# Kernel tuning notes

Hardware: AMD Instinct MI355X
Metric: run time of the kernel (lower is better)

The kernel has to match this reference:

```python
import jax, jax.numpy as jnp
import numpy as np

B, HH, WW, C, HEADS = 8, 56, 56, 384, 6
DIM_OUT = 384


def _upsample2x_bilinear(x):
    # x: [..., m, n] -> [..., 2m, 2n]; matches torch F.interpolate bilinear align_corners=False
    m, n = x.shape[-2], x.shape[-1]
    def coords(inn):
        c = (jnp.arange(2 * inn) + 0.5) / 2.0 - 0.5
        c = jnp.clip(c, 0.0, inn - 1)
        i0 = jnp.floor(c).astype(jnp.int32)
        i1 = jnp.minimum(i0 + 1, inn - 1)
        return i0, i1, (c - i0).astype(x.dtype)
    i0, i1, wy = coords(m)
    j0, j1, wx = coords(n)
    rows = x[..., i0, :] * (1 - wy)[:, None] + x[..., i1, :] * wy[:, None]
    return rows[..., :, j0] * (1 - wx) + rows[..., :, j1] * wx


def setup_inputs() -> dict:
    key = jax.random.key(0)
    ks = jax.random.split(key, 12)
    inp = {
        'x': jax.random.normal(ks[0], (B, HH * WW, C), jnp.float32),
        'res_attn': jax.random.normal(ks[1], (B, HEADS, (HH // 4) * (WW // 4), (HH // 2) * (WW // 2)), jnp.float32),
        'conv_q_w': jax.random.normal(ks[2], (C, 1, 3, 3), jnp.float32) * 0.05,
        'ln_g': jnp.ones((C,), jnp.float32),
        'ln_b': jnp.zeros((C,), jnp.float32),
        'wq': jax.random.normal(ks[3], (DIM_OUT, C), jnp.float32) * 0.02,
        'wk': jax.random.normal(ks[4], (DIM_OUT, C), jnp.float32) * 0.02,
        'wv': jax.random.normal(ks[5], (DIM_OUT, C), jnp.float32) * 0.02,
        'w_proj': jax.random.normal(ks[6], (DIM_OUT, DIM_OUT), jnp.float32) * 0.02,
        'b_proj': jnp.zeros((DIM_OUT,), jnp.float32),
        'w_fuse': jax.random.normal(ks[7], (HEADS, 2 * HEADS, 1, 1), jnp.float32) * 0.1,
        'b_fuse': jnp.zeros((HEADS,), jnp.float32),
        'h': HH,
        'w': WW,
    }
    return inp


def reference(x, res_attn, conv_q_w, ln_g, ln_b, wq, wk, wv, w_proj, b_proj, w_fuse, b_fuse, h, w):
    Bz, _, Cc = x.shape
    heads = w_fuse.shape[0]
    xi = x.transpose(0, 2, 1).reshape(Bz, Cc, h, w)  # b c h w
    # conv_proj_q: depthwise conv k3 s2 p1 (no bias), then LayerNorm
    q = jax.lax.conv_general_dilated(
        xi, conv_q_w, (2, 2), ((1, 1), (1, 1)),
        dimension_numbers=('NCHW', 'OIHW', 'NCHW'), feature_group_count=Cc)
    hq, wq2 = q.shape[2], q.shape[3]
    q = q.reshape(Bz, Cc, hq * wq2).transpose(0, 2, 1)  # b t c
    mu = q.mean(-1, keepdims=True)
    var = ((q - mu) ** 2).mean(-1, keepdims=True)
    q = (q - mu) / jnp.sqrt(var + 1e-5) * ln_g + ln_b
    # conv_proj_k/v: avg pool k2 s2 p0
    kv = xi.reshape(Bz, Cc, h // 2, 2, w // 2, 2).mean(axis=(3, 5))
    kv = kv.reshape(Bz, Cc, (h // 2) * (w // 2)).transpose(0, 2, 1)  # b t c
    dim_out = wq.shape[0]
    dh = dim_out // heads
    def split(t):
        return t.reshape(Bz, t.shape[1], heads, dh).transpose(0, 2, 1, 3)
    qh = split(q @ wq.T)
    kh = split(kv @ wk.T)
    vh = split(kv @ wv.T)
    scale = dim_out ** -0.5
    attn_score = jnp.einsum('bhlk,bhtk->bhlt', qh, kh) * scale  # [B,H,L,T]
    sh, sw = h // 4, w // 4
    a = res_attn.shape[-1]
    rx = res_attn[:, :, :sh * sw, :]
    rx = rx.reshape(Bz * heads, sh * sw, a).transpose(0, 2, 1).reshape(Bz * heads, a, sh, sw)
    rx = _upsample2x_bilinear(rx)  # (b h) a 2sh 2sw
    rx = rx.reshape(Bz, heads, a, 4 * sh * sw).transpose(0, 1, 3, 2)  # b h L a
    cat = jnp.concatenate([attn_score, rx], axis=1)  # [B, 2H, L, T]
    attn_score = jnp.einsum('bclt,oc->bolt', cat, w_fuse[:, :, 0, 0]) + b_fuse[None, :, None, None]
    attn = jax.nn.softmax(attn_score, axis=-1)
    out = jnp.einsum('bhlt,bhtv->bhlv', attn, vh)
    out = out.transpose(0, 2, 1, 3).reshape(Bz, -1, dim_out)
    return out @ w_proj.T + b_proj
```

## Files before the change

kernel.cpp:

```cpp
#include <hip/hip_runtime.h>

typedef unsigned int uint;
typedef unsigned short ushort_t;
typedef short bf16x8 __attribute__((ext_vector_type(8)));
typedef float f32x4 __attribute__((ext_vector_type(4)));

__device__ __forceinline__ ushort_t f2bf(float f) {
  uint u = __builtin_bit_cast(uint, f);
  u += 0x7fffu + ((u >> 16) & 1u);
  return (ushort_t)(u >> 16);
}
__device__ __forceinline__ float bf2f(ushort_t s) {
  return __builtin_bit_cast(float, (uint)s << 16);
}
__device__ __forceinline__ bf16x8 ld_frag(const ushort_t* p) {
  return __builtin_bit_cast(bf16x8, *(const uint4*)p);
}

__global__ __launch_bounds__(384) void k_convln(
    const float* __restrict__ x, const float* __restrict__ wc,
    const float* __restrict__ g, const float* __restrict__ bb,
    ushort_t* __restrict__ qout, ushort_t* __restrict__ kvout)
{
  const int b  = blockIdx.x / 784;
  const int t  = blockIdx.x % 784;
  const int oy = t / 28, ox = t % 28;
  const int c  = threadIdx.x;
  const float* xb = x + (size_t)b * 3136 * 384 + c;
  float acc = 0.f, pv = 0.f;
  #pragma unroll
  for (int ky = 0; ky < 3; ky++) {
    const int iy = 2 * oy - 1 + ky;
    const bool yok = (iy >= 0) & (iy < 56);
    #pragma unroll
    for (int kx = 0; kx < 3; kx++) {
      const int ix = 2 * ox - 1 + kx;
      if (yok & (ix >= 0) & (ix < 56)) {
        const float xv = xb[(size_t)(iy * 56 + ix) * 384];
        acc += wc[c * 9 + ky * 3 + kx] * xv;
        if ((ky >= 1) & (kx >= 1)) pv += xv;
      }
    }
  }
  kvout[((size_t)b * 784 + t) * 384 + c] = f2bf(pv * 0.25f);
  float s = acc, s2 = acc * acc;
  #pragma unroll
  for (int off = 32; off >= 1; off >>= 1) {
    s  += __shfl_xor(s,  off);
    s2 += __shfl_xor(s2, off);
  }
  __shared__ float ps[6], ps2[6];
  if ((c & 63) == 0) { ps[c >> 6] = s; ps2[c >> 6] = s2; }
  __syncthreads();
  float S = 0.f, S2 = 0.f;
  #pragma unroll
  for (int i = 0; i < 6; i++) { S += ps[i]; S2 += ps2[i]; }
  const float mu  = S * (1.f / 384.f);
  const float var = S2 * (1.f / 384.f) - mu * mu;
  const float inv = rsqrtf(var + 1e-5f);
  qout[((size_t)b * 784 + t) * 384 + c] = f2bf((acc - mu) * inv * g[c] + bb[c]);
}

__global__ __launch_bounds__(256) void k_wcvt(
    const float* __restrict__ a, const float* __restrict__ b,
    const float* __restrict__ c, const float* __restrict__ d,
    ushort_t* __restrict__ oa, ushort_t* __restrict__ ob,
    ushort_t* __restrict__ oc, ushort_t* __restrict__ od)
{
  const int i = blockIdx.x * 256 + threadIdx.x;
  if (i < 147456) {
    oa[i] = f2bf(a[i]); ob[i] = f2bf(b[i]);
    oc[i] = f2bf(c[i]); od[i] = f2bf(d[i]);
  }
}

template<int MODE>
__global__ __launch_bounds__(256) void k_gemm(
    const ushort_t* __restrict__ X, const ushort_t* __restrict__ W,
    const float* __restrict__ bias, void* __restrict__ Y)
{
  __shared__ ushort_t As[128][40];
  __shared__ ushort_t Bs[128][40];
  const int tid = threadIdx.x, w = tid >> 6, lane = tid & 63;
  const int quad = lane >> 4, r = lane & 15;
  const int m0 = blockIdx.y * 128, n0 = blockIdx.x * 128;
  const int wm = w >> 1, wn = w & 1;
  const int lr = tid >> 2, lc = (tid & 3) << 3;
  const ushort_t* xp = X + (size_t)(m0 + lr) * 384 + lc;
  const ushort_t* wp = W + (size_t)(n0 + lr) * 384 + lc;
  f32x4 acc[4][4] = {};
  for (int k0 = 0; k0 < 384; k0 += 32) {
    __syncthreads();
    *(uint4*)&As[lr][lc]      = *(const uint4*)(xp + k0);
    *(uint4*)&As[lr + 64][lc] = *(const uint4*)(xp + (size_t)64 * 384 + k0);
    *(uint4*)&Bs[lr][lc]      = *(const uint4*)(wp + k0);
    *(uint4*)&Bs[lr + 64][lc] = *(const uint4*)(wp + (size_t)64 * 384 + k0);
    __syncthreads();
    bf16x8 af[4], bf_[4];
    #pragma unroll
    for (int mt = 0; mt < 4; mt++) af[mt]  = *(const bf16x8*)&As[wm * 64 + mt * 16 + r][quad * 8];
    #pragma unroll
    for (int nt = 0; nt < 4; nt++) bf_[nt] = *(const bf16x8*)&Bs[wn * 64 + nt * 16 + r][quad * 8];
    #pragma unroll
    for (int mt = 0; mt < 4; mt++)
      #pragma unroll
      for (int nt = 0; nt < 4; nt++)
        acc[mt][nt] = __builtin_amdgcn_mfma_f32_16x16x32_bf16(af[mt], bf_[nt], acc[mt][nt], 0, 0, 0);
  }
  #pragma unroll
  for (int mt = 0; mt < 4; mt++) {
    #pragma unroll
    for (int nt = 0; nt < 4; nt++) {
      #pragma unroll
      for (int i = 0; i < 4; i++) {
        const int row = m0 + wm * 64 + mt * 16 + quad * 4 + i;
        const int col = n0 + wn * 64 + nt * 16 + r;
        const float v = acc[mt][nt][i];
        if constexpr (MODE == 2) {
          ((float*)Y)[(size_t)row * 384 + col] = v + bias[col];
        } else if constexpr (MODE == 0) {
          ((ushort_t*)Y)[(size_t)row * 384 + col] = f2bf(v);
        } else {
          const int bb = row / 784, tt = row % 784;
          ((ushort_t*)Y)[((size_t)bb * 384 + col) * 784 + tt] = f2bf(v);
        }
      }
    }
  }
}

__global__ __launch_bounds__(256) void k_qk(
    const ushort_t* __restrict__ Qb, const ushort_t* __restrict__ Kb,
    ushort_t* __restrict__ S)
{
  const int tid = threadIdx.x, w = tid >> 6, lane = tid & 63;
  const int quad = lane >> 4, r = lane & 15;
  const int bh = blockIdx.z, b = bh / 6, h = bh % 6;
  const int m0 = blockIdx.y * 64 + w * 16;
  const int t0 = blockIdx.x * 112;
  const int lq = min(m0 + r, 783);
  const ushort_t* qp = Qb + (size_t)(b * 784 + lq) * 384 + h * 64 + quad * 8;
  const bf16x8 a0 = ld_frag(qp), a1 = ld_frag(qp + 32);
  f32x4 acc[7] = {};
  #pragma unroll
  for (int j = 0; j < 7; j++) {
    const int t = t0 + j * 16 + r;
    const ushort_t* kp = Kb + (size_t)(b * 784 + t) * 384 + h * 64 + quad * 8;
    acc[j] = __builtin_amdgcn_mfma_f32_16x16x32_bf16(a0, ld_frag(kp),      acc[j], 0, 0, 0);
    acc[j] = __builtin_amdgcn_mfma_f32_16x16x32_bf16(a1, ld_frag(kp + 32), acc[j], 0, 0, 0);
  }
  const float scale = 0.05103103630798288f;
  #pragma unroll
  for (int j = 0; j < 7; j++) {
    #pragma unroll
    for (int i = 0; i < 4; i++) {
      const int lo = m0 + quad * 4 + i;
      if (lo < 784)
        S[((size_t)(b * 784 + lo) * 6 + h) * 784 + t0 + j * 16 + r] = f2bf(acc[j][i] * scale);
    }
  }
}

__global__ __launch_bounds__(256) void k_fuse(
    ushort_t* __restrict__ S, const float* __restrict__ ra,
    const float* __restrict__ w_fuse, const float* __restrict__ b_fuse)
{
  const int tid = threadIdx.x;
  const int bl = blockIdx.x, b = bl / 784, l = bl % 784;
  __shared__ float wf[72], bfu[6];
  __shared__ float reds[4][6];
  if (tid < 72) wf[tid] = w_fuse[tid];
  if (tid < 6)  bfu[tid] = b_fuse[tid];
  __syncthreads();

  const int Y = l / 28, X = l % 28;
  const float cy = fminf(fmaxf((float)Y * 0.5f - 0.25f, 0.f), 13.f);
  const float cx = fminf(fmaxf((float)X * 0.5f - 0.25f, 0.f), 13.f);
  const int y0 = (int)cy, y1 = min(y0 + 1, 13);
  const int x0 = (int)cx, x1 = min(x0 + 1, 13);
  const float fy = cy - (float)y0, fx = cx - (float)x0;
  const float w00 = (1.f - fy) * (1.f - fx), w01 = (1.f - fy) * fx;
  const float w10 = fy * (1.f - fx),         w11 = fy * fx;
  const int p00 = (y0 * 14 + x0) * 784, p01 = (y0 * 14 + x1) * 784;
  const int p10 = (y1 * 14 + x0) * 784, p11 = (y1 * 14 + x1) * 784;

  ushort_t* Srow = S + (size_t)bl * 6 * 784;
  const float* rab = ra + (size_t)b * 6 * 196 * 784;

  float F[4][6];
  float sm[6] = {};
  #pragma unroll
  for (int j = 0; j < 4; j++) {
    const int t = tid + j * 256;
    if (t < 784) {
      float a[6];
      #pragma unroll
      for (int o = 0; o < 6; o++) a[o] = bfu[o];
      #pragma unroll
      for (int c = 0; c < 6; c++) {
        const float* rc = rab + (size_t)c * (196 * 784);
        const float rx = w00 * rc[p00 + t] + w01 * rc[p01 + t]
                       + w10 * rc[p10 + t] + w11 * rc[p11 + t];
        const float sv = bf2f(Srow[c * 784 + t]);
        #pragma unroll
        for (int o = 0; o < 6; o++) a[o] += wf[o * 12 + c] * sv + wf[o * 12 + 6 + c] * rx;
      }
      #pragma unroll
      for (int o = 0; o < 6; o++) {
        const float p = __expf(fminf(a[o], 60.f));
        F[j][o] = p; sm[o] += p;
      }
    } else {
      #pragma unroll
      for (int o = 0; o < 6; o++) F[j][o] = 0.f;
    }
  }
  #pragma unroll
  for (int o = 0; o < 6; o++) {
    #pragma unroll
    for (int off = 32; off >= 1; off >>= 1) sm[o] += __shfl_xor(sm[o], off);
  }
  if ((tid & 63) == 0) {
    #pragma unroll
    for (int o = 0; o < 6; o++) reds[tid >> 6][o] = sm[o];
  }
  __syncthreads();
  float inv[6];
  #pragma unroll
  for (int o = 0; o < 6; o++)
    inv[o] = 1.f / (reds[0][o] + reds[1][o] + reds[2][o] + reds[3][o]);
  #pragma unroll
  for (int j = 0; j < 4; j++) {
    const int t = tid + j * 256;
    if (t < 784) {
      #pragma unroll
      for (int o = 0; o < 6; o++) Srow[o * 784 + t] = f2bf(F[j][o] * inv[o]);
    }
  }
}

__global__ __launch_bounds__(256) void k_pv(
    const ushort_t* __restrict__ P, const ushort_t* __restrict__ Vt,
    ushort_t* __restrict__ O)
{
  const int tid = threadIdx.x, w = tid >> 6, lane = tid & 63;
  const int quad = lane >> 4, r = lane & 15;
  const int bo = blockIdx.y, b = bo / 6, o = bo % 6;
  const int m0 = blockIdx.x * 64 + w * 16;
  const int lq = min(m0 + r, 783);
  const ushort_t* ap = P + ((size_t)(b * 784 + lq) * 6 + o) * 784 + quad * 8;
  const ushort_t* bp = Vt + ((size_t)b * 384 + o * 64 + r) * 784 + quad * 8;
  f32x4 acc[4] = {};
  for (int kk = 0; kk < 25; kk++) {
    const int k0 = kk * 32;
    const bool full = (kk < 24) | (quad < 2);
    bf16x8 af = {}, bf_[4] = {};
    if (full) {
      af = ld_frag(ap + k0);
      #pragma unroll
      for (int nt = 0; nt < 4; nt++) bf_[nt] = ld_frag(bp + (size_t)nt * 16 * 784 + k0);
    }
    #pragma unroll
    for (int nt = 0; nt < 4; nt++)
      acc[nt] = __builtin_amdgcn_mfma_f32_16x16x32_bf16(af, bf_[nt], acc[nt], 0, 0, 0);
  }
  #pragma unroll
  for (int nt = 0; nt < 4; nt++) {
    #pragma unroll
    for (int i = 0; i < 4; i++) {
      const int lo = m0 + quad * 4 + i;
      if (lo < 784)
        O[(size_t)(b * 784 + lo) * 384 + o * 64 + nt * 16 + r] = f2bf(acc[nt][i]);
    }
  }
}

extern "C" void kernel_launch(void* const* d_in, const int* in_sizes, int n_in,
                              void* d_out, int out_size, void* d_ws, size_t ws_size,
                              hipStream_t stream)
{
  const float* x        = (const float*)d_in[0];
  const float* res_attn = (const float*)d_in[1];
  const float* conv_w   = (const float*)d_in[2];
  const float* ln_g     = (const float*)d_in[3];
  const float* ln_b     = (const float*)d_in[4];
  const float* wq       = (const float*)d_in[5];
  const float* wk       = (const float*)d_in[6];
  const float* wv       = (const float*)d_in[7];
  const float* w_proj   = (const float*)d_in[8];
  const float* b_proj   = (const float*)d_in[9];
  const float* w_fuse   = (const float*)d_in[10];
  const float* b_fuse   = (const float*)d_in[11];
  float* out = (float*)d_out;

  const size_t NE = (size_t)8 * 784 * 384;
  const size_t NW = 147456;
  ushort_t* q_ln_b = (ushort_t*)d_ws;
  ushort_t* kv_b   = q_ln_b + NE;
  ushort_t* Qb     = kv_b + NE;
  ushort_t* Kb     = Qb + NE;
  ushort_t* Vt     = Kb + NE;
  ushort_t* Opre   = Vt + NE;
  ushort_t* wqb    = Opre + NE;
  ushort_t* wkb    = wqb + NW;
  ushort_t* wvb    = wkb + NW;
  ushort_t* wpb    = wvb + NW;
  ushort_t* S      = wpb + NW;

  k_convln<<<dim3(8 * 784), dim3(384), 0, stream>>>(x, conv_w, ln_g, ln_b, q_ln_b, kv_b);
  k_wcvt  <<<dim3(576),     dim3(256), 0, stream>>>(wq, wk, wv, w_proj, wqb, wkb, wvb, wpb);

  k_gemm<0><<<dim3(3, 49), dim3(256), 0, stream>>>(q_ln_b, wqb, nullptr, Qb);
  k_gemm<0><<<dim3(3, 49), dim3(256), 0, stream>>>(kv_b,   wkb, nullptr, Kb);
  k_gemm<1><<<dim3(3, 49), dim3(256), 0, stream>>>(kv_b,   wvb, nullptr, Vt);

  k_qk  <<<dim3(7, 13, 48), dim3(256), 0, stream>>>(Qb, Kb, S);
  k_fuse<<<dim3(8 * 784),   dim3(256), 0, stream>>>(S, res_attn, w_fuse, b_fuse);
  k_pv  <<<dim3(13, 48),    dim3(256), 0, stream>>>(S, Vt, Opre);

  k_gemm<2><<<dim3(3, 49), dim3(256), 0, stream>>>(Opre, wpb, b_proj, out);
}
```

Before: 319.6 us.

## Fuse QK scores with head-mix fusion and defer softmax normalization to PV

Merges the Q, K and V projection GEMMs into one launch over a z-dimension. Replaces the separate QK-score and fuse/softmax kernels with a single kernel. That kernel computes all six heads' scores in registers, applies the bilinear residual mix and the 1x1 head-fusion conv, and writes unnormalized exp values. The PV kernel then sums the P rows it loads and divides the output by that sum. This removes the bf16 score write/read round trip and a whole 6272-block launch. The trade-off is that the exp is taken without a max-subtraction (only a clamp at 60), and the row sum is accumulated from bf16-rounded P values.

```diff
diff --git a/kernel.cpp b/kernel.cpp
--- a/kernel.cpp
+++ b/kernel.cpp
@@ -74,10 +74,68 @@
   }
 }
 
-template<int MODE>
-__global__ __launch_bounds__(256) void k_gemm(
+__global__ __launch_bounds__(256) void k_gemm3(
+    const ushort_t* __restrict__ Xq, const ushort_t* __restrict__ Xkv,
+    const ushort_t* __restrict__ Wq, const ushort_t* __restrict__ Wk,
+    const ushort_t* __restrict__ Wv,
+    ushort_t* __restrict__ Qo, ushort_t* __restrict__ Ko,
+    ushort_t* __restrict__ Vo)
+{
+  __shared__ ushort_t As[128][40];
+  __shared__ ushort_t Bs[128][40];
+  const int z = blockIdx.z;
+  const ushort_t* X = (z == 0) ? Xq : Xkv;
+  const ushort_t* W = (z == 0) ? Wq : (z == 1) ? Wk : Wv;
+  const int tid = threadIdx.x, w = tid >> 6, lane = tid & 63;
+  const int quad = lane >> 4, r = lane & 15;
+  const int m0 = blockIdx.y * 128, n0 = blockIdx.x * 128;
+  const int wm = w >> 1, wn = w & 1;
+  const int lr = tid >> 2, lc = (tid & 3) << 3;
+  const ushort_t* xp = X + (size_t)(m0 + lr) * 384 + lc;
+  const ushort_t* wp = W + (size_t)(n0 + lr) * 384 + lc;
+  f32x4 acc[4][4] = {};
+  for (int k0 = 0; k0 < 384; k0 += 32) {
+    __syncthreads();
+    *(uint4*)&As[lr][lc]      = *(const uint4*)(xp + k0);
+    *(uint4*)&As[lr + 64][lc] = *(const uint4*)(xp + (size_t)64 * 384 + k0);
+    *(uint4*)&Bs[lr][lc]      = *(const uint4*)(wp + k0);
+    *(uint4*)&Bs[lr + 64][lc] = *(const uint4*)(wp + (size_t)64 * 384 + k0);
+    __syncthreads();
+    bf16x8 af[4], bf_[4];
+    #pragma unroll
+    for (int mt = 0; mt < 4; mt++) af[mt]  = *(const bf16x8*)&As[wm * 64 + mt * 16 + r][quad * 8];
+    #pragma unroll
+    for (int nt = 0; nt < 4; nt++) bf_[nt] = *(const bf16x8*)&Bs[wn * 64 + nt * 16 + r][quad * 8];
+    #pragma unroll
+    for (int mt = 0; mt < 4; mt++)
+      #pragma unroll
+      for (int nt = 0; nt < 4; nt++)
+        acc[mt][nt] = __builtin_amdgcn_mfma_f32_16x16x32_bf16(af[mt], bf_[nt], acc[mt][nt], 0, 0, 0);
+  }
+  #pragma unroll
+  for (int mt = 0; mt < 4; mt++) {
+    #pragma unroll
+    for (int nt = 0; nt < 4; nt++) {
+      #pragma unroll
+      for (int i = 0; i < 4; i++) {
+        const int row = m0 + wm * 64 + mt * 16 + quad * 4 + i;
+        const int col = n0 + wn * 64 + nt * 16 + r;
+        const float v = acc[mt][nt][i];
+        if (z < 2) {
+          ushort_t* Y = (z == 0) ? Qo : Ko;
+          Y[(size_t)row * 384 + col] = f2bf(v);
+        } else {
+          const int bb = row / 784, tt = row % 784;
+          Vo[((size_t)bb * 384 + col) * 784 + tt] = f2bf(v);
+        }
+      }
+    }
+  }
+}
+
+__global__ __launch_bounds__(256) void k_gemmo(
     const ushort_t* __restrict__ X, const ushort_t* __restrict__ W,
-    const float* __restrict__ bias, void* __restrict__ Y)
+    const float* __restrict__ bias, float* __restrict__ Y)
 {
   __shared__ ushort_t As[128][40];
   __shared__ ushort_t Bs[128][40];
@@ -115,131 +173,100 @@
       for (int i = 0; i < 4; i++) {
         const int row = m0 + wm * 64 + mt * 16 + quad * 4 + i;
         const int col = n0 + wn * 64 + nt * 16 + r;
-        const float v = acc[mt][nt][i];
-        if constexpr (MODE == 2) {
-          ((float*)Y)[(size_t)row * 384 + col] = v + bias[col];
-        } else if constexpr (MODE == 0) {
-          ((ushort_t*)Y)[(size_t)row * 384 + col] = f2bf(v);
-        } else {
-          const int bb = row / 784, tt = row % 784;
-          ((ushort_t*)Y)[((size_t)bb * 384 + col) * 784 + tt] = f2bf(v);
+        Y[(size_t)row * 384 + col] = acc[mt][nt][i] + bias[col];
+      }
+    }
+  }
+}
+
+__global__ __launch_bounds__(256) void k_qkfuse(
+    const ushort_t* __restrict__ Qb, const ushort_t* __restrict__ Kb,
+    const float* __restrict__ ra, const float* __restrict__ w_fuse,
+    const float* __restrict__ b_fuse, ushort_t* __restrict__ P)
+{
+  const int tid = threadIdx.x, w = tid >> 6, lane = tid & 63;
+  const int quad = lane >> 4, r = lane & 15;
+  const int b  = blockIdx.z;
+  const int m0 = blockIdx.y * 64 + w * 16;
+  const int t0 = blockIdx.x * 32;
+
+  __shared__ float wf[72], bfu[6];
+  if (tid < 72) wf[tid] = w_fuse[tid] * ((tid % 12) < 6 ? 0.05103103630798288f : 1.f);
+  if (tid < 6)  bfu[tid] = b_fuse[tid];
+  __syncthreads();
+
+  const int lq = min(m0 + r, 783);
+  const ushort_t* qp = Qb + (size_t)(b * 784 + lq) * 384 + quad * 8;
+  bf16x8 qf[6][2];
+  #pragma unroll
+  for (int h = 0; h < 6; h++) {
+    qf[h][0] = ld_frag(qp + h * 64);
+    qf[h][1] = ld_frag(qp + h * 64 + 32);
+  }
+  f32x4 acc[6][2] = {};
+  #pragma unroll
+  for (int j = 0; j < 2; j++) {
+    const int t = min(t0 + j * 16 + r, 783);
+    const ushort_t* kp = Kb + (size_t)(b * 784 + t) * 384 + quad * 8;
+    #pragma unroll
+    for (int h = 0; h < 6; h++) {
+      acc[h][j] = __builtin_amdgcn_mfma_f32_16x16x32_bf16(
+          qf[h][0], ld_frag(kp + h * 64),      acc[h][j], 0, 0, 0);
+      acc[h][j] = __builtin_amdgcn_mfma_f32_16x16x32_bf16(
+          qf[h][1], ld_frag(kp + h * 64 + 32), acc[h][j], 0, 0, 0);
+    }
+  }
+
+  int p00a[4], p01a[4], p10a[4], p11a[4];
+  float w00a[4], w01a[4], w10a[4], w11a[4];
+  #pragma unroll
+  for (int i = 0; i < 4; i++) {
+    const int l = min(m0 + quad * 4 + i, 783);
+    const int Y = l / 28, X = l % 28;
+    const float cy = fminf(fmaxf((float)Y * 0.5f - 0.25f, 0.f), 13.f);
+    const float cx = fminf(fmaxf((float)X * 0.5f - 0.25f, 0.f), 13.f);
+    const int y0 = (int)cy, y1 = min(y0 + 1, 13);
+    const int x0 = (int)cx, x1 = min(x0 + 1, 13);
+    const float fy = cy - (float)y0, fx = cx - (float)x0;
+    w00a[i] = (1.f - fy) * (1.f - fx); w01a[i] = (1.f - fy) * fx;
+    w10a[i] = fy * (1.f - fx);         w11a[i] = fy * fx;
+    p00a[i] = (y0 * 14 + x0) * 784; p01a[i] = (y0 * 14 + x1) * 784;
+    p10a[i] = (y1 * 14 + x0) * 784; p11a[i] = (y1 * 14 + x1) * 784;
+  }
+  const float* rab = ra + (size_t)b * 6 * 153664;
+
+  #pragma unroll
+  for (int j = 0; j < 2; j++) {
+    const int t = t0 + j * 16 + r;
+    if (t < 784) {
+      #pragma unroll
+      for (int i = 0; i < 4; i++) {
+        const int lo = m0 + quad * 4 + i;
+        if (lo < 784) {
+          float a[6];
+          #pragma unroll
+          for (int o = 0; o < 6; o++) a[o] = bfu[o];
+          #pragma unroll
+          for (int c = 0; c < 6; c++) {
+            const float* rc = rab + (size_t)c * 153664;
+            const float rx = w00a[i] * rc[p00a[i] + t] + w01a[i] * rc[p01a[i] + t]
+                           + w10a[i] * rc[p10a[i] + t] + w11a[i] * rc[p11a[i] + t];
+            const float sv = acc[c][j][i];
+            #pragma unroll
+            for (int o = 0; o < 6; o++)
+              a[o] += wf[o * 12 + c] * sv + wf[o * 12 + 6 + c] * rx;
+          }
+          ushort_t* prow = P + ((size_t)(b * 784 + lo) * 6) * 784 + t;
+          #pragma unroll
+          for (int o = 0; o < 6; o++)
+            prow[(size_t)o * 784] = f2bf(__expf(fminf(a[o], 60.f)));
         }
       }
     }
   }
 }
 
-__global__ __launch_bounds__(256) void k_qk(
-    const ushort_t* __restrict__ Qb, const ushort_t* __restrict__ Kb,
-    ushort_t* __restrict__ S)
-{
-  const int tid = threadIdx.x, w = tid >> 6, lane = tid & 63;
-  const int quad = lane >> 4, r = lane & 15;
-  const int bh = blockIdx.z, b = bh / 6, h = bh % 6;
-  const int m0 = blockIdx.y * 64 + w * 16;
-  const int t0 = blockIdx.x * 112;
-  const int lq = min(m0 + r, 783);
-  const ushort_t* qp = Qb + (size_t)(b * 784 + lq) * 384 + h * 64 + quad * 8;
-  const bf16x8 a0 = ld_frag(qp), a1 = ld_frag(qp + 32);
-  f32x4 acc[7] = {};
-  #pragma unroll
-  for (int j = 0; j < 7; j++) {
-    const int t = t0 + j * 16 + r;
-    const ushort_t* kp = Kb + (size_t)(b * 784 + t) * 384 + h * 64 + quad * 8;
-    acc[j] = __builtin_amdgcn_mfma_f32_16x16x32_bf16(a0, ld_frag(kp),      acc[j], 0, 0, 0);
-    acc[j] = __builtin_amdgcn_mfma_f32_16x16x32_bf16(a1, ld_frag(kp + 32), acc[j], 0, 0, 0);
-  }
-  const float scale = 0.05103103630798288f;
-  #pragma unroll
-  for (int j = 0; j < 7; j++) {
-    #pragma unroll
-    for (int i = 0; i < 4; i++) {
-      const int lo = m0 + quad * 4 + i;
-      if (lo < 784)
-        S[((size_t)(b * 784 + lo) * 6 + h) * 784 + t0 + j * 16 + r] = f2bf(acc[j][i] * scale);
-    }
-  }
-}
-
-__global__ __launch_bounds__(256) void k_fuse(
-    ushort_t* __restrict__ S, const float* __restrict__ ra,
-    const float* __restrict__ w_fuse, const float* __restrict__ b_fuse)
-{
-  const int tid = threadIdx.x;
-  const int bl = blockIdx.x, b = bl / 784, l = bl % 784;
-  __shared__ float wf[72], bfu[6];
-  __shared__ float reds[4][6];
-  if (tid < 72) wf[tid] = w_fuse[tid];
-  if (tid < 6)  bfu[tid] = b_fuse[tid];
-  __syncthreads();
-
-  const int Y = l / 28, X = l % 28;
-  const float cy = fminf(fmaxf((float)Y * 0.5f - 0.25f, 0.f), 13.f);
-  const float cx = fminf(fmaxf((float)X * 0.5f - 0.25f, 0.f), 13.f);
-  const int y0 = (int)cy, y1 = min(y0 + 1, 13);
-  const int x0 = (int)cx, x1 = min(x0 + 1, 13);
-  const float fy = cy - (float)y0, fx = cx - (float)x0;
-  const float w00 = (1.f - fy) * (1.f - fx), w01 = (1.f - fy) * fx;
-  const float w10 = fy * (1.f - fx),         w11 = fy * fx;
-  const int p00 = (y0 * 14 + x0) * 784, p01 = (y0 * 14 + x1) * 784;
-  const int p10 = (y1 * 14 + x0) * 784, p11 = (y1 * 14 + x1) * 784;
-
-  ushort_t* Srow = S + (size_t)bl * 6 * 784;
-  const float* rab = ra + (size_t)b * 6 * 196 * 784;
-
-  float F[4][6];
-  float sm[6] = {};
-  #pragma unroll
-  for (int j = 0; j < 4; j++) {
-    const int t = tid + j * 256;
-    if (t < 784) {
-      float a[6];
-      #pragma unroll
-      for (int o = 0; o < 6; o++) a[o] = bfu[o];
-      #pragma unroll
-      for (int c = 0; c < 6; c++) {
-        const float* rc = rab + (size_t)c * (196 * 784);
-        const float rx = w00 * rc[p00 + t] + w01 * rc[p01 + t]
-                       + w10 * rc[p10 + t] + w11 * rc[p11 + t];
-        const float sv = bf2f(Srow[c * 784 + t]);
-        #pragma unroll
-        for (int o = 0; o < 6; o++) a[o] += wf[o * 12 + c] * sv + wf[o * 12 + 6 + c] * rx;
-      }
-      #pragma unroll
-      for (int o = 0; o < 6; o++) {
-        const float p = __expf(fminf(a[o], 60.f));
-        F[j][o] = p; sm[o] += p;
-      }
-    } else {
-      #pragma unroll
-      for (int o = 0; o < 6; o++) F[j][o] = 0.f;
-    }
-  }
-  #pragma unroll
-  for (int o = 0; o < 6; o++) {
-    #pragma unroll
-    for (int off = 32; off >= 1; off >>= 1) sm[o] += __shfl_xor(sm[o], off);
-  }
-  if ((tid & 63) == 0) {
-    #pragma unroll
-    for (int o = 0; o < 6; o++) reds[tid >> 6][o] = sm[o];
-  }
-  __syncthreads();
-  float inv[6];
-  #pragma unroll
-  for (int o = 0; o < 6; o++)
-    inv[o] = 1.f / (reds[0][o] + reds[1][o] + reds[2][o] + reds[3][o]);
-  #pragma unroll
-  for (int j = 0; j < 4; j++) {
-    const int t = tid + j * 256;
-    if (t < 784) {
-      #pragma unroll
-      for (int o = 0; o < 6; o++) Srow[o * 784 + t] = f2bf(F[j][o] * inv[o]);
-    }
-  }
-}
-
-__global__ __launch_bounds__(256) void k_pv(
+__global__ __launch_bounds__(256) void k_pvs(
     const ushort_t* __restrict__ P, const ushort_t* __restrict__ Vt,
     ushort_t* __restrict__ O)
 {
@@ -251,12 +278,16 @@
   const ushort_t* ap = P + ((size_t)(b * 784 + lq) * 6 + o) * 784 + quad * 8;
   const ushort_t* bp = Vt + ((size_t)b * 384 + o * 64 + r) * 784 + quad * 8;
   f32x4 acc[4] = {};
+  float ps = 0.f;
   for (int kk = 0; kk < 25; kk++) {
     const int k0 = kk * 32;
     const bool full = (kk < 24) | (quad < 2);
     bf16x8 af = {}, bf_[4] = {};
     if (full) {
       af = ld_frag(ap + k0);
+      const ushort_t* sv = (const ushort_t*)&af;
+      #pragma unroll
+      for (int e = 0; e < 8; e++) ps += bf2f(sv[e]);
       #pragma unroll
       for (int nt = 0; nt < 4; nt++) bf_[nt] = ld_frag(bp + (size_t)nt * 16 * 784 + k0);
     }
@@ -264,13 +295,19 @@
     for (int nt = 0; nt < 4; nt++)
       acc[nt] = __builtin_amdgcn_mfma_f32_16x16x32_bf16(af, bf_[nt], acc[nt], 0, 0, 0);
   }
+  ps += __shfl_xor(ps, 16);
+  ps += __shfl_xor(ps, 32);
+  float inv[4];
+  #pragma unroll
+  for (int i = 0; i < 4; i++) inv[i] = 1.f / __shfl(ps, quad * 4 + i);
   #pragma unroll
   for (int nt = 0; nt < 4; nt++) {
     #pragma unroll
     for (int i = 0; i < 4; i++) {
       const int lo = m0 + quad * 4 + i;
       if (lo < 784)
-        O[(size_t)(b * 784 + lo) * 384 + o * 64 + nt * 16 + r] = f2bf(acc[nt][i]);
+        O[(size_t)(b * 784 + lo) * 384 + o * 64 + nt * 16 + r] =
+            f2bf(acc[nt][i] * inv[i]);
     }
   }
 }
@@ -305,18 +342,17 @@
   ushort_t* wkb    = wqb + NW;
   ushort_t* wvb    = wkb + NW;
   ushort_t* wpb    = wvb + NW;
-  ushort_t* S      = wpb + NW;
+  ushort_t* P      = wpb + NW;
 
   k_convln<<<dim3(8 * 784), dim3(384), 0, stream>>>(x, conv_w, ln_g, ln_b, q_ln_b, kv_b);
   k_wcvt  <<<dim3(576),     dim3(256), 0, stream>>>(wq, wk, wv, w_proj, wqb, wkb, wvb, wpb);
 
-  k_gemm<0><<<dim3(3, 49), dim3(256), 0, stream>>>(q_ln_b, wqb, nullptr, Qb);
-  k_gemm<0><<<dim3(3, 49), dim3(256), 0, stream>>>(kv_b,   wkb, nullptr, Kb);
-  k_gemm<1><<<dim3(3, 49), dim3(256), 0, stream>>>(kv_b,   wvb, nullptr, Vt);
-
-  k_qk  <<<dim3(7, 13, 48), dim3(256), 0, stream>>>(Qb, Kb, S);
-  k_fuse<<<dim3(8 * 784),   dim3(256), 0, stream>>>(S, res_attn, w_fuse, b_fuse);
-  k_pv  <<<dim3(13, 48),    dim3(256), 0, stream>>>(S, Vt, Opre);
-
-  k_gemm<2><<<dim3(3, 49), dim3(256), 0, stream>>>(Opre, wpb, b_proj, out);
-}
+  k_gemm3<<<dim3(3, 49, 3), dim3(256), 0, stream>>>(
+      q_ln_b, kv_b, wqb, wkb, wvb, Qb, Kb, Vt);
+
+  k_qkfuse<<<dim3(25, 13, 8), dim3(256), 0, stream>>>(
+      Qb, Kb, res_attn, w_fuse, b_fuse, P);
+  k_pvs<<<dim3(13, 48), dim3(256), 0, stream>>>(P, Vt, Opre);
+
+  k_gemmo<<<dim3(3, 49), dim3(256), 0, stream>>>(Opre, wpb, b_proj, out);
+}
```

Result: slower. 339.6 us (+6.3%).
